# Kernel optimization log

Hardware: AMD Instinct MI355X
Metric: run time of the kernel (lower is better)

## Reference

```python
import jax, jax.numpy as jnp
import numpy as np

N = 16384   # src points
M = 16384   # ref points
D = 256     # d_embed
K = 16      # num_neighbors
MAX_DIST = 0.5


def _knn(src, ref, k):
    # squared euclidean distances, [N, M] (pytorch3d knn_points returns squared dists)
    d2 = (jnp.sum(src * src, axis=-1, keepdims=True)
          + jnp.sum(ref * ref, axis=-1)[None, :]
          - 2.0 * src @ ref.T)
    neg_d2, idx = jax.lax.top_k(-d2, k)   # k smallest distances, sorted ascending
    return -neg_d2, idx


def setup_inputs() -> dict:
    key = jax.random.key(0)
    k1, k2, k3, k4, k5 = jax.random.split(key, 5)
    return {
        "ref_points": jax.random.normal(k1, (M, 3), dtype=jnp.float32),
        "src_points": jax.random.normal(k2, (N, 3), dtype=jnp.float32),
        "ref_feats": jax.random.normal(k3, (M, D), dtype=jnp.float32),
        "src_feats": jax.random.normal(k4, (N, D), dtype=jnp.float32),
        "W": jax.random.normal(k5, (D, D), dtype=jnp.float32) * 0.1,
    }


def reference(ref_points, src_points, ref_feats, src_feats, W):
    dist, knn_idx = _knn(src_points, ref_points, K)      # [N,K], [N,K]
    knn_xyz = ref_points[knn_idx]                        # [N,K,3]
    weight = jax.nn.relu(1.0 - dist / MAX_DIST)          # [N,K]

    W_triu = jnp.triu(W)
    W_sym = W_triu + W_triu.T                            # symmetric bilinear form
    knn_feats = ref_feats[knn_idx]                       # [N,K,D]

    scores = jnp.einsum('nc,cd,nkd->nk', src_feats, W_sym, knn_feats)
    attn = jax.nn.softmax(scores * weight, axis=-1)      # [N,K]
    corres = jnp.einsum('nk,nkc->nc', attn, knn_xyz)     # [N,3]

    d = jnp.linalg.norm(src_points - corres, axis=-1)    # [N]
    w = jax.nn.relu(1.0 - d / MAX_DIST)                  # [N]
    return corres, w
```

## Files before the change

### kernel.cpp

```cpp
#include <hip/hip_runtime.h>
#include <math.h>

#define N_SRC 16384
#define M_REF 16384
#define DEMB  256
#define KNN_K 16
#define CAP   128

__global__ void wsym_kernel(const float* __restrict__ W, float* __restrict__ wsym) {
    int i = blockIdx.x;
    int j = threadIdx.x;
    float a = (j >= i) ? W[i * DEMB + j] : 0.f;
    float b = (i >= j) ? W[j * DEMB + i] : 0.f;
    wsym[i * DEMB + j] = a + b;
}

__global__ void pack_kernel(const float* __restrict__ rp, float4* __restrict__ out) {
    int i = blockIdx.x * 256 + threadIdx.x;
    float x = rp[i * 3 + 0], y = rp[i * 3 + 1], z = rp[i * 3 + 2];
    out[i] = make_float4(x, y, z, fmaf(x, x, fmaf(y, y, z * z)));
}

__global__ void __launch_bounds__(256) q_kernel(const float* __restrict__ src_feats,
                                                const float* __restrict__ wsym,
                                                float* __restrict__ q) {
    __shared__ __align__(16) float sf[16][DEMB];
    int n0 = blockIdx.x * 16;
    int tid = threadIdx.x;
    int c0 = tid & 63;
    int rg = tid >> 6;
    {
        int c = c0 * 4;
        #pragma unroll
        for (int rr = 0; rr < 4; ++rr) {
            int r = rr * 4 + rg;
            *(float4*)&sf[r][c] = *(const float4*)&src_feats[(size_t)(n0 + r) * DEMB + c];
        }
    }
    __syncthreads();

    float acc[4][4];
    #pragma unroll
    for (int rr = 0; rr < 4; ++rr)
        #pragma unroll
        for (int cc = 0; cc < 4; ++cc) acc[rr][cc] = 0.f;

    for (int c4 = 0; c4 < 64; ++c4) {
        float wv[4][4];
        #pragma unroll
        for (int j = 0; j < 4; ++j)
            #pragma unroll
            for (int cc = 0; cc < 4; ++cc)
                wv[j][cc] = wsym[(size_t)(c4 * 4 + j) * DEMB + c0 + cc * 64];
        #pragma unroll
        for (int rr = 0; rr < 4; ++rr) {
            float4 s = *(const float4*)&sf[rg * 4 + rr][c4 * 4];
            #pragma unroll
            for (int cc = 0; cc < 4; ++cc) {
                float a = acc[rr][cc];
                a = fmaf(s.x, wv[0][cc], a);
                a = fmaf(s.y, wv[1][cc], a);
                a = fmaf(s.z, wv[2][cc], a);
                a = fmaf(s.w, wv[3][cc], a);
                acc[rr][cc] = a;
            }
        }
    }
    #pragma unroll
    for (int rr = 0; rr < 4; ++rr)
        #pragma unroll
        for (int cc = 0; cc < 4; ++cc)
            q[(size_t)(n0 + rg * 4 + rr) * DEMB + (c0 + cc * 64)] = acc[rr][cc];
}

__device__ __forceinline__ void sort64_kv(float& vd, int& vi, int lane) {
    #pragma unroll
    for (int k = 2; k <= 64; k <<= 1) {
        #pragma unroll
        for (int j = k >> 1; j > 0; j >>= 1) {
            float od = __shfl_xor(vd, j, 64);
            int   oi = __shfl_xor(vi, j, 64);
            bool keep_min = (((lane & j) == 0) == ((lane & k) == 0));
            bool oless = (od < vd) || (od == vd && oi < vi);
            bool take = (keep_min == oless);
            vd = take ? od : vd;
            vi = take ? oi : vi;
        }
    }
}

__global__ void __launch_bounds__(256) knn_kernel(const float* __restrict__ src_points,
                                                  const float4* __restrict__ refp4,
                                                  float* __restrict__ kd2,
                                                  int* __restrict__ kidx) {
    const float INF = 3.0e38f;
    int tid = threadIdx.x;
    int wave = tid >> 6, lane = tid & 63;
    int g = wave & 1, h = wave >> 1;
    int n0 = blockIdx.x * 16 + g * 8;

    __shared__ float cd[2][8][CAP];
    __shared__ int   ci[2][8][CAP];
    __shared__ int   cnt[2][8];
    if (tid < 16) cnt[tid >> 3][tid & 7] = 0;

    float m2x[8], m2y[8], m2z[8], sn2[8];
    #pragma unroll
    for (int b = 0; b < 8; ++b) {
        float sx = src_points[(n0 + b) * 3 + 0];
        float sy = src_points[(n0 + b) * 3 + 1];
        float sz = src_points[(n0 + b) * 3 + 2];
        m2x[b] = -2.f * sx; m2y[b] = -2.f * sy; m2z[b] = -2.f * sz;
        sn2[b] = fmaf(sx, sx, fmaf(sy, sy, sz * sz));
    }
    __syncthreads();

    const int base = h * (M_REF / 2);

    float mind[8];
    #pragma unroll
    for (int b = 0; b < 8; ++b) mind[b] = INF;
    for (int it = 0; it < 128; it += 2) {
        float4 r0 = refp4[base + it * 64 + lane];
        float4 r1 = refp4[base + (it + 1) * 64 + lane];
        #pragma unroll
        for (int b = 0; b < 8; ++b) {
            float d0 = fmaf(r0.x, m2x[b], r0.w);
            d0 = fmaf(r0.y, m2y[b], d0);
            d0 = fmaf(r0.z, m2z[b], d0);
            float d1 = fmaf(r1.x, m2x[b], r1.w);
            d1 = fmaf(r1.y, m2y[b], d1);
            d1 = fmaf(r1.z, m2z[b], d1);
            mind[b] = fminf(mind[b], fminf(d0, d1));
        }
    }

    float tau[8];
    #pragma unroll
    for (int b = 0; b < 8; ++b) {
        float v = mind[b];
        #pragma unroll
        for (int k = 2; k <= 64; k <<= 1) {
            #pragma unroll
            for (int j = k >> 1; j > 0; j >>= 1) {
                float o = __shfl_xor(v, j, 64);
                bool lower = (lane & j) == 0;
                bool up = (lane & k) == 0;
                float mn = fminf(v, o), mx = fmaxf(v, o);
                v = (lower == up) ? mn : mx;
            }
        }
        tau[b] = __shfl(v, 15, 64);
    }

    for (int it = 0; it < 128; it += 2) {
        int i0 = base + it * 64 + lane;
        float4 r0 = refp4[i0];
        float4 r1 = refp4[i0 + 64];
        #pragma unroll
        for (int b = 0; b < 8; ++b) {
            float d0 = fmaf(r0.x, m2x[b], r0.w);
            d0 = fmaf(r0.y, m2y[b], d0);
            d0 = fmaf(r0.z, m2z[b], d0);
            float d1 = fmaf(r1.x, m2x[b], r1.w);
            d1 = fmaf(r1.y, m2y[b], d1);
            d1 = fmaf(r1.z, m2z[b], d1);
            if (d0 <= tau[b]) {
                int p = atomicAdd(&cnt[g][b], 1);
                if (p < CAP) { cd[g][b][p] = d0; ci[g][b][p] = i0; }
            }
            if (d1 <= tau[b]) {
                int p = atomicAdd(&cnt[g][b], 1);
                if (p < CAP) { cd[g][b][p] = d1; ci[g][b][p] = i0 + 64; }
            }
        }
    }
    __syncthreads();

    #pragma unroll
    for (int bb = 0; bb < 4; ++bb) {
        int b = h * 4 + bb;
        int count = cnt[g][b];
        if (count > CAP) count = CAP;
        float vd = (lane < count) ? cd[g][b][lane] : INF;
        int   vi = (lane < count) ? ci[g][b][lane] : 0x7fffffff;
        sort64_kv(vd, vi, lane);
        int done = 64;
        while (done < count) {
            if (lane >= 16) {
                int p = done + (lane - 16);
                vd = (p < count) ? cd[g][b][p] : INF;
                vi = (p < count) ? ci[g][b][p] : 0x7fffffff;
            }
            sort64_kv(vd, vi, lane);
            done += 48;
        }
        if (lane < KNN_K) {
            kd2[(size_t)(n0 + b) * KNN_K + lane] = vd + sn2[b];
            kidx[(size_t)(n0 + b) * KNN_K + lane] = vi;
        }
    }
}

__global__ void __launch_bounds__(256) score_kernel(const float* __restrict__ q,
                                                    const float* __restrict__ ref_feats,
                                                    const float* __restrict__ ref_points,
                                                    const float* __restrict__ src_points,
                                                    const float* __restrict__ kd2,
                                                    const int* __restrict__ kidx,
                                                    float* __restrict__ out) {
    int wave = threadIdx.x >> 6;
    int lane = threadIdx.x & 63;
    int n = blockIdx.x * 4 + wave;

    float4 qv = *(const float4*)&q[(size_t)n * DEMB + lane * 4];

    int idx[KNN_K]; float d2[KNN_K];
    #pragma unroll
    for (int k = 0; k < KNN_K; ++k) {
        idx[k] = kidx[(size_t)n * KNN_K + k];
        d2[k]  = kd2[(size_t)n * KNN_K + k];
    }

    float sc[KNN_K];
    #pragma unroll
    for (int k = 0; k < KNN_K; ++k) {
        float4 r = *(const float4*)&ref_feats[(size_t)idx[k] * DEMB + lane * 4];
        float p = fmaf(r.x, qv.x, fmaf(r.y, qv.y, fmaf(r.z, qv.z, r.w * qv.w)));
        #pragma unroll
        for (int off = 1; off < 64; off <<= 1) p += __shfl_xor(p, off, 64);
        sc[k] = p;
    }

    float tv[KNN_K];
    #pragma unroll
    for (int k = 0; k < KNN_K; ++k) {
        float wt = fmaxf(0.f, fmaf(-2.f, d2[k], 1.f));
        tv[k] = sc[k] * wt;
    }
    float m = tv[0];
    #pragma unroll
    for (int k = 1; k < KNN_K; ++k) m = fmaxf(m, tv[k]);
    float e[KNN_K], s = 0.f;
    #pragma unroll
    for (int k = 0; k < KNN_K; ++k) { e[k] = expf(tv[k] - m); s += e[k]; }

    float cx = 0.f, cy = 0.f, cz = 0.f;
    #pragma unroll
    for (int k = 0; k < KNN_K; ++k) {
        float rx = ref_points[idx[k] * 3 + 0];
        float ry = ref_points[idx[k] * 3 + 1];
        float rz = ref_points[idx[k] * 3 + 2];
        cx = fmaf(e[k], rx, cx);
        cy = fmaf(e[k], ry, cy);
        cz = fmaf(e[k], rz, cz);
    }
    float inv = 1.f / s;
    cx *= inv; cy *= inv; cz *= inv;

    if (lane == 0) {
        float ssx = src_points[n * 3 + 0];
        float ssy = src_points[n * 3 + 1];
        float ssz = src_points[n * 3 + 2];
        float dx = ssx - cx, dy = ssy - cy, dz = ssz - cz;
        float dist = sqrtf(fmaf(dx, dx, fmaf(dy, dy, dz * dz)));
        float w = fmaxf(0.f, fmaf(-2.f, dist, 1.f));
        out[(size_t)n * 3 + 0] = cx;
        out[(size_t)n * 3 + 1] = cy;
        out[(size_t)n * 3 + 2] = cz;
        out[(size_t)N_SRC * 3 + n] = w;
    }
}

extern "C" void kernel_launch(void* const* d_in, const int* in_sizes, int n_in,
                              void* d_out, int out_size, void* d_ws, size_t ws_size,
                              hipStream_t stream) {
    const float* ref_points = (const float*)d_in[0];
    const float* src_points = (const float*)d_in[1];
    const float* ref_feats  = (const float*)d_in[2];
    const float* src_feats  = (const float*)d_in[3];
    const float* W          = (const float*)d_in[4];
    float* out = (float*)d_out;

    float*  wsym  = (float*)d_ws;
    float4* refp4 = (float4*)(wsym + DEMB * DEMB);
    float*  q     = (float*)(refp4 + M_REF);
    float*  kd2   = q + (size_t)N_SRC * DEMB;
    int*    kidx  = (int*)(kd2 + (size_t)N_SRC * KNN_K);

    wsym_kernel<<<DEMB, DEMB, 0, stream>>>(W, wsym);
    pack_kernel<<<M_REF / 256, 256, 0, stream>>>(ref_points, refp4);
    q_kernel<<<N_SRC / 16, 256, 0, stream>>>(src_feats, wsym, q);
    knn_kernel<<<N_SRC / 16, 256, 0, stream>>>(src_points, refp4, kd2, kidx);
    score_kernel<<<N_SRC / 4, 256, 0, stream>>>(q, ref_feats, ref_points, src_points, kd2, kidx, out);
}
```

Before: 172.1 us.

## Enlarge q tile, shrink knn blocks, scalarize score neighbor indices

The q GEMM kernel now computes 32 rows per block instead of 16, so each W_sym load is reused across twice as many rows at the cost of more accumulator registers. The knn kernel drops to 128-thread blocks handling 8 source points each, which gives more and smaller blocks with less shared memory per block. The score kernel passes the row and neighbor indices through readfirstlane so the gather addresses become wave-uniform scalars.

```diff
diff --git a/kernel.cpp b/kernel.cpp
--- a/kernel.cpp
+++ b/kernel.cpp
@@ -24,24 +24,24 @@
 __global__ void __launch_bounds__(256) q_kernel(const float* __restrict__ src_feats,
                                                 const float* __restrict__ wsym,
                                                 float* __restrict__ q) {
-    __shared__ __align__(16) float sf[16][DEMB];
-    int n0 = blockIdx.x * 16;
+    __shared__ __align__(16) float sf[32][DEMB];
+    int n0 = blockIdx.x * 32;
     int tid = threadIdx.x;
     int c0 = tid & 63;
     int rg = tid >> 6;
     {
         int c = c0 * 4;
         #pragma unroll
-        for (int rr = 0; rr < 4; ++rr) {
+        for (int rr = 0; rr < 8; ++rr) {
             int r = rr * 4 + rg;
             *(float4*)&sf[r][c] = *(const float4*)&src_feats[(size_t)(n0 + r) * DEMB + c];
         }
     }
     __syncthreads();
 
-    float acc[4][4];
-    #pragma unroll
-    for (int rr = 0; rr < 4; ++rr)
+    float acc[8][4];
+    #pragma unroll
+    for (int rr = 0; rr < 8; ++rr)
         #pragma unroll
         for (int cc = 0; cc < 4; ++cc) acc[rr][cc] = 0.f;
 
@@ -53,8 +53,8 @@
             for (int cc = 0; cc < 4; ++cc)
                 wv[j][cc] = wsym[(size_t)(c4 * 4 + j) * DEMB + c0 + cc * 64];
         #pragma unroll
-        for (int rr = 0; rr < 4; ++rr) {
-            float4 s = *(const float4*)&sf[rg * 4 + rr][c4 * 4];
+        for (int rr = 0; rr < 8; ++rr) {
+            float4 s = *(const float4*)&sf[rg * 8 + rr][c4 * 4];
             #pragma unroll
             for (int cc = 0; cc < 4; ++cc) {
                 float a = acc[rr][cc];
@@ -67,10 +67,10 @@
         }
     }
     #pragma unroll
-    for (int rr = 0; rr < 4; ++rr)
+    for (int rr = 0; rr < 8; ++rr)
         #pragma unroll
         for (int cc = 0; cc < 4; ++cc)
-            q[(size_t)(n0 + rg * 4 + rr) * DEMB + (c0 + cc * 64)] = acc[rr][cc];
+            q[(size_t)(n0 + rg * 8 + rr) * DEMB + (c0 + cc * 64)] = acc[rr][cc];
 }
 
 __device__ __forceinline__ void sort64_kv(float& vd, int& vi, int lane) {
@@ -89,20 +89,19 @@
     }
 }
 
-__global__ void __launch_bounds__(256) knn_kernel(const float* __restrict__ src_points,
+__global__ void __launch_bounds__(128) knn_kernel(const float* __restrict__ src_points,
                                                   const float4* __restrict__ refp4,
                                                   float* __restrict__ kd2,
                                                   int* __restrict__ kidx) {
     const float INF = 3.0e38f;
     int tid = threadIdx.x;
-    int wave = tid >> 6, lane = tid & 63;
-    int g = wave & 1, h = wave >> 1;
-    int n0 = blockIdx.x * 16 + g * 8;
-
-    __shared__ float cd[2][8][CAP];
-    __shared__ int   ci[2][8][CAP];
-    __shared__ int   cnt[2][8];
-    if (tid < 16) cnt[tid >> 3][tid & 7] = 0;
+    int h = tid >> 6, lane = tid & 63;
+    int n0 = blockIdx.x * 8;
+
+    __shared__ float cd[8][CAP];
+    __shared__ int   ci[8][CAP];
+    __shared__ int   cnt[8];
+    if (tid < 8) cnt[tid] = 0;
 
     float m2x[8], m2y[8], m2z[8], sn2[8];
     #pragma unroll
@@ -166,12 +165,12 @@
             d1 = fmaf(r1.y, m2y[b], d1);
             d1 = fmaf(r1.z, m2z[b], d1);
             if (d0 <= tau[b]) {
-                int p = atomicAdd(&cnt[g][b], 1);
-                if (p < CAP) { cd[g][b][p] = d0; ci[g][b][p] = i0; }
+                int p = atomicAdd(&cnt[b], 1);
+                if (p < CAP) { cd[b][p] = d0; ci[b][p] = i0; }
             }
             if (d1 <= tau[b]) {
-                int p = atomicAdd(&cnt[g][b], 1);
-                if (p < CAP) { cd[g][b][p] = d1; ci[g][b][p] = i0 + 64; }
+                int p = atomicAdd(&cnt[b], 1);
+                if (p < CAP) { cd[b][p] = d1; ci[b][p] = i0 + 64; }
             }
         }
     }
@@ -180,17 +179,17 @@
     #pragma unroll
     for (int bb = 0; bb < 4; ++bb) {
         int b = h * 4 + bb;
-        int count = cnt[g][b];
+        int count = cnt[b];
         if (count > CAP) count = CAP;
-        float vd = (lane < count) ? cd[g][b][lane] : INF;
-        int   vi = (lane < count) ? ci[g][b][lane] : 0x7fffffff;
+        float vd = (lane < count) ? cd[b][lane] : INF;
+        int   vi = (lane < count) ? ci[b][lane] : 0x7fffffff;
         sort64_kv(vd, vi, lane);
         int done = 64;
         while (done < count) {
             if (lane >= 16) {
                 int p = done + (lane - 16);
-                vd = (p < count) ? cd[g][b][p] : INF;
-                vi = (p < count) ? ci[g][b][p] : 0x7fffffff;
+                vd = (p < count) ? cd[b][p] : INF;
+                vi = (p < count) ? ci[b][p] : 0x7fffffff;
             }
             sort64_kv(vd, vi, lane);
             done += 48;
@@ -211,14 +210,14 @@
                                                     float* __restrict__ out) {
     int wave = threadIdx.x >> 6;
     int lane = threadIdx.x & 63;
-    int n = blockIdx.x * 4 + wave;
+    int n = __builtin_amdgcn_readfirstlane(blockIdx.x * 4 + wave);
 
     float4 qv = *(const float4*)&q[(size_t)n * DEMB + lane * 4];
 
     int idx[KNN_K]; float d2[KNN_K];
     #pragma unroll
     for (int k = 0; k < KNN_K; ++k) {
-        idx[k] = kidx[(size_t)n * KNN_K + k];
+        idx[k] = __builtin_amdgcn_readfirstlane(kidx[(size_t)n * KNN_K + k]);
         d2[k]  = kd2[(size_t)n * KNN_K + k];
     }
 
@@ -290,7 +289,7 @@
 
     wsym_kernel<<<DEMB, DEMB, 0, stream>>>(W, wsym);
     pack_kernel<<<M_REF / 256, 256, 0, stream>>>(ref_points, refp4);
-    q_kernel<<<N_SRC / 16, 256, 0, stream>>>(src_feats, wsym, q);
-    knn_kernel<<<N_SRC / 16, 256, 0, stream>>>(src_points, refp4, kd2, kidx);
+    q_kernel<<<N_SRC / 32, 256, 0, stream>>>(src_feats, wsym, q);
+    knn_kernel<<<N_SRC / 8, 128, 0, stream>>>(src_points, refp4, kd2, kidx);
     score_kernel<<<N_SRC / 4, 256, 0, stream>>>(q, ref_feats, ref_points, src_points, kd2, kidx, out);
 }
```

Result: slower. 176.4 us (+2.4%).
